# Performance work log

Hardware: AMD Instinct MI355X
Metric: run time of the kernel (lower is better)

The kernel has to match this reference:

```python
import jax, jax.numpy as jnp
import numpy as np
from math import factorial, sqrt

L_MAX = 3
MUL = 64
# e3nn FullyConnectedTensorProduct instruction order: lexicographic over (l1, l2, l3)
# keeping paths with triangle inequality and matching parity ((-1)^(l1+l2) == (-1)^l3).
PATHS = [(l1, l2, l3)
         for l1 in range(L_MAX + 1)
         for l2 in range(L_MAX + 1)
         for l3 in range(L_MAX + 1)
         if abs(l1 - l2) <= l3 <= l1 + l2 and (l1 + l2 + l3) % 2 == 0]
assert len(PATHS) == 23
N_TO = {l3: sum(1 for p in PATHS if p[2] == l3) for l3 in range(L_MAX + 1)}


def _su2_cg(j1, m1, j2, m2, j3, m3):
    # Complex-basis Clebsch-Gordan coefficient (Racah formula), as in e3nn.
    if m3 != m1 + m2:
        return 0.0
    f = factorial
    vmin = max(-j1 + j2 + m3, -j1 + m1, 0)
    vmax = min(j2 + j3 + m1, j3 - j1 + j2, j3 + m3)
    c = sqrt((2 * j3 + 1) * f(j3 + j1 - j2) * f(j3 - j1 + j2) * f(j1 + j2 - j3)
             * f(j3 + m3) * f(j3 - m3)
             / (f(j1 + j2 + j3 + 1) * f(j1 - m1) * f(j1 + m1) * f(j2 - m2) * f(j2 + m2)))
    s = 0.0
    for v in range(vmin, vmax + 1):
        s += (-1) ** (v + j2 + m2) / f(v) * f(j2 + j3 + m1 - v) * f(j1 - m1 + v) \
             / f(j3 - j1 + j2 - v) / f(j3 + m3 - v) / f(v + j1 - j2 - m3)
    return c * s


def _q(l):
    # Change of basis real -> complex spherical harmonics (e3nn convention).
    q = np.zeros((2 * l + 1, 2 * l + 1), dtype=np.complex128)
    for m in range(-l, 0):
        q[l + m, l + abs(m)] = 1.0 / np.sqrt(2.0)
        q[l + m, l - abs(m)] = -1j / np.sqrt(2.0)
    q[l, l] = 1.0
    for m in range(1, l + 1):
        q[l + m, l + abs(m)] = (-1) ** m / np.sqrt(2.0)
        q[l + m, l - abs(m)] = 1j * (-1) ** m / np.sqrt(2.0)
    return (-1j) ** l * q


def _w3j(l1, l2, l3):
    # Real-basis Wigner 3j tensor, unit Frobenius norm (e3nn's o3.wigner_3j).
    csu2 = np.zeros((2 * l1 + 1, 2 * l2 + 1, 2 * l3 + 1))
    for m1 in range(-l1, l1 + 1):
        for m2 in range(-l2, l2 + 1):
            m3 = m1 + m2
            if -l3 <= m3 <= l3:
                csu2[l1 + m1, l2 + m2, l3 + m3] = _su2_cg(l1, m1, l2, m2, l3, m3)
    q1, q2, q3 = _q(l1), _q(l2), _q(l3)
    c = np.einsum('ij,kl,mn,ikn->jlm', q1, q2, np.conj(q3.T), csu2.astype(np.complex128))
    c = np.real(c)
    return (c / np.linalg.norm(c)).astype(np.float32)


W3J = {p: jnp.asarray(_w3j(*p)) for p in PATHS}
# e3nn 'component' irrep_normalization + 'element' path_normalization:
# per-path coeff = sqrt(ir_out.dim / (n_paths_into_out * mul1 * mul2)).
COEFF = {p: float(np.sqrt((2 * p[2] + 1) / (N_TO[p[2]] * MUL * MUL))) for p in PATHS}


def setup_inputs():
    key = jax.random.key(0)
    kx, kw = jax.random.split(key)
    x = jax.random.normal(kx, (2, 1024, MUL * (L_MAX + 1) ** 2), dtype=jnp.float32)
    weights = jax.random.normal(kw, (len(PATHS), MUL, MUL, MUL), dtype=jnp.float32)
    return {"x": x, "weights": weights}


def reference(x, weights):
    B, N, D = x.shape
    Z = B * N
    xf = x.reshape(Z, D)
    # e3nn layout: blocks of (mul, 2l+1) concatenated over l; offset = MUL * l^2.
    xs = [xf[:, MUL * l * l: MUL * (l + 1) ** 2].reshape(Z, MUL, 2 * l + 1)
          for l in range(L_MAX + 1)]
    acc = [jnp.zeros((Z, MUL, 2 * l + 1), dtype=x.dtype) for l in range(L_MAX + 1)]
    for p, (l1, l2, l3) in enumerate(PATHS):
        c = W3J[(l1, l2, l3)]
        t1 = jnp.einsum('zui,ijk->zujk', xs[l1], c)            # [Z,u,2l2+1,2l3+1]
        t2 = jnp.einsum('zujk,zvj->zuvk', t1, xs[l2])          # [Z,u,v,2l3+1]
        seg = jnp.einsum('zuvk,uvw->zwk', t2, weights[p]) * COEFF[(l1, l2, l3)]
        acc[l3] = acc[l3] + seg
    out = jnp.concatenate([a.reshape(Z, -1) for a in acc], axis=-1)
    return out.reshape(B, N, -1)
```

## Files before the change

kernel.cpp:

```cpp
#include <hip/hip_runtime.h>

struct CD { double re, im; };
constexpr CD cmul(CD a, CD b){ return CD{a.re*b.re - a.im*b.im, a.re*b.im + a.im*b.re}; }
constexpr CD conj_(CD a){ return CD{a.re, -a.im}; }

constexpr double factd(int n){ double r = 1.0; for(int i = 2; i <= n; ++i) r *= (double)i; return r; }
constexpr double csqrt_(double x){
  if (x <= 0.0) return 0.0;
  double g = x > 1.0 ? x : 1.0;
  for (int i = 0; i < 100; ++i) g = 0.5*(g + x/g);
  return g;
}

constexpr double su2_cg(int j1,int m1,int j2,int m2,int j3,int m3){
  if (m3 != m1 + m2) return 0.0;
  int vmin = -j1 + j2 + m3;
  if (-j1 + m1 > vmin) vmin = -j1 + m1;
  if (0 > vmin) vmin = 0;
  int vmax = j2 + j3 + m1;
  if (j3 - j1 + j2 < vmax) vmax = j3 - j1 + j2;
  if (j3 + m3 < vmax) vmax = j3 + m3;
  double c = csqrt_((2.0*j3 + 1.0) * factd(j3 + j1 - j2) * factd(j3 - j1 + j2) * factd(j1 + j2 - j3)
                    * factd(j3 + m3) * factd(j3 - m3)
                    / (factd(j1 + j2 + j3 + 1) * factd(j1 - m1) * factd(j1 + m1)
                       * factd(j2 - m2) * factd(j2 + m2)));
  double s = 0.0;
  for (int v = vmin; v <= vmax; ++v){
    double t = (((v + j2 + m2) & 1) ? -1.0 : 1.0) / factd(v)
               * factd(j2 + j3 + m1 - v) * factd(j1 - m1 + v)
               / factd(j3 - j1 + j2 - v) / factd(j3 + m3 - v) / factd(v + j1 - j2 - m3);
    s += t;
  }
  return c * s;
}

struct QM { CD m[7][7]; };
constexpr QM qmat(int l){
  QM q{};
  double is2 = 1.0 / csqrt_(2.0);
  for (int mm = -l; mm < 0; ++mm){
    q.m[l+mm][l-mm] = CD{is2, 0.0};
    q.m[l+mm][l+mm] = CD{0.0, -is2};
  }
  q.m[l][l] = CD{1.0, 0.0};
  for (int mm = 1; mm <= l; ++mm){
    double sgn = (mm & 1) ? -1.0 : 1.0;
    q.m[l+mm][l+mm] = CD{sgn*is2, 0.0};
    q.m[l+mm][l-mm] = CD{0.0, sgn*is2};
  }
  CD ph = (l % 4 == 0) ? CD{1,0} : (l % 4 == 1) ? CD{0,-1} : (l % 4 == 2) ? CD{-1,0} : CD{0,1};
  for (int r = 0; r < 7; ++r)
    for (int c = 0; c < 7; ++c)
      q.m[r][c] = cmul(ph, q.m[r][c]);
  return q;
}

template<int L1,int L2,int L3> struct W3JT { float v[2*L1+1][2*L2+1][2*L3+1]; };

template<int L1,int L2,int L3>
constexpr W3JT<L1,L2,L3> make_w3j(){
  constexpr int D1 = 2*L1+1, D2 = 2*L2+1, D3 = 2*L3+1;
  QM q1 = qmat(L1), q2 = qmat(L2), q3 = qmat(L3);
  double cg[7][7] = {};
  for (int i = 0; i < D1; ++i)
    for (int k = 0; k < D2; ++k){
      int n = i + k - L1 - L2 + L3;
      if (n >= 0 && n < D3) cg[i][k] = su2_cg(L1, i-L1, L2, k-L2, L3, (i-L1)+(k-L2));
    }
  double c[D1][D2][D3] = {};
  double norm2 = 0.0;
  for (int j = 0; j < D1; ++j)
    for (int l = 0; l < D2; ++l)
      for (int m = 0; m < D3; ++m){
        CD s{0.0, 0.0};
        for (int i = 0; i < D1; ++i)
          for (int k = 0; k < D2; ++k){
            double g = cg[i][k];
            if (g == 0.0) continue;
            int n = i + k - L1 - L2 + L3;
            CD t = cmul(q1.m[i][j], q2.m[k][l]);
            t = cmul(t, conj_(q3.m[n][m]));
            s.re += t.re * g; s.im += t.im * g;
          }
        c[j][l][m] = s.re;
        norm2 += s.re * s.re;
      }
  double inv = 1.0 / csqrt_(norm2);
  W3JT<L1,L2,L3> w{};
  for (int j = 0; j < D1; ++j)
    for (int l = 0; l < D2; ++l)
      for (int m = 0; m < D3; ++m){
        double val = c[j][l][m] * inv;
        if (val < 1e-10 && val > -1e-10) val = 0.0;
        w.v[j][l][m] = (float)val;
      }
  return w;
}

__device__ __constant__ int L3P_[23]  = {0,1,2,3,1,0,2,1,3,2,2,1,3,0,2,1,3,3,2,1,3,0,2};
__device__ __constant__ int SWAPP_[23] = {0,1,1,1,0,0,0,1,1,1,0,0,0,0,0,1,1,0,0,0,0,0,0};
constexpr int K3CUM[24] = {0,1,4,9,16,19,20,25,28,35,40,45,48,55,56,61,64,71,78,83,86,93,94,99};
constexpr size_t ZW = 2048ull * 64ull;

typedef __bf16 bf16x8 __attribute__((ext_vector_type(8)));
typedef float  f32x4  __attribute__((ext_vector_type(4)));
typedef float  f32x2  __attribute__((ext_vector_type(2)));

__global__ void pack_w_kernel(const float* __restrict__ w, unsigned short* __restrict__ wp, int total){
  int idx = blockIdx.x * 256 + threadIdx.x;
  if (idx >= total) return;
  int e    = idx & 7;
  int lane = (idx >> 3) & 63;
  int nt   = (idx >> 9) & 3;
  int hf   = (idx >> 11) & 1;
  int s    = (idx >> 12) & 63;
  int p    = idx >> 18;
  int kv = hf*32 + (lane >> 4)*8 + e;
  int wc = nt*16 + (lane & 15);
  int l3 = L3P_[p];
  const float nto[4] = {4.f, 6.f, 7.f, 6.f};
  float coeff = sqrtf((2.f*l3 + 1.f) / (nto[l3] * 4096.f));
  int a = SWAPP_[p] ? kv : s;
  int b = SWAPP_[p] ? s : kv;
  float val = w[(((size_t)p*64 + a)*64 + b)*64 + wc] * coeff;
  unsigned bits = __builtin_bit_cast(unsigned, val);
  unsigned r = (bits + 0x7FFFu + ((bits >> 16) & 1u)) >> 16;
  wp[idx] = (unsigned short)r;
}

__global__ void transpose_x(const float* __restrict__ x, float* __restrict__ xT){
  __shared__ float t[32][33];
  int bx = blockIdx.x, by = blockIdx.y;
  int tx = threadIdx.x & 31, ty = threadIdx.x >> 5;
  #pragma unroll
  for (int r = 0; r < 4; ++r)
    t[ty + r*8][tx] = x[(size_t)(by*32 + ty + r*8)*1024 + bx*32 + tx];
  __syncthreads();
  #pragma unroll
  for (int r = 0; r < 4; ++r)
    xT[(size_t)(bx*32 + ty + r*8)*2048 + by*32 + tx] = t[tx][ty + r*8];
}

template<int P,int L1,int L2,int L3,bool SWAP,int G0,int G,bool PART>
__device__ __forceinline__ void run_slot(
    int tile, const float* __restrict__ xT,
    const unsigned short* __restrict__ wp,
    float* __restrict__ dst, float* red)
{
  constexpr int K3 = 2*L3+1;
  constexpr int LK = SWAP ? L1 : L2;
  constexpr int LS = SWAP ? L2 : L1;
  constexpr int DK = 2*LK+1, DS = 2*LS+1;
  constexpr auto C = make_w3j<L1,L2,L3>();

  const int lane = threadIdx.x & 63;
  const int wv   = threadIdx.x >> 6;
  const int zc   = tile*16 + (lane & 15);

  f32x2 xk2[4][DK];
  {
    const float* xkb = xT + (size_t)(64*LK*LK)*2048 + zc;
    const int t0 = wv*32 + (lane >> 4)*8;
    #pragma unroll
    for (int q = 0; q < 4; ++q)
      #pragma unroll
      for (int t = 0; t < DK; ++t){
        float lo = xkb[(size_t)((t0 + 2*q    )*DK + t)*2048];
        float hi = xkb[(size_t)((t0 + 2*q + 1)*DK + t)*2048];
        xk2[q][t] = f32x2{lo, hi};
      }
  }

  const float* xsb = xT + (size_t)(64*LS*LS)*2048 + zc;
  const unsigned short* wu = wp + (size_t)P*262144 + (size_t)wv*2048 + (size_t)lane*8;

  f32x4 acc[G][4];
  #pragma unroll
  for (int a = 0; a < G; ++a)
    #pragma unroll
    for (int b = 0; b < 4; ++b) acc[a][b] = f32x4{0.f,0.f,0.f,0.f};

  const float* xsp = xsb;
  float xs[DS];
  #pragma unroll
  for (int j = 0; j < DS; ++j) xs[j] = xsp[(size_t)j*2048];

  for (int s = 0; s < 64; ++s){
    bf16x8 bfrag[4];
    #pragma unroll
    for (int nt = 0; nt < 4; ++nt)
      bfrag[nt] = *reinterpret_cast<const bf16x8*>(wu + nt*512);

    const float* xnp = (s < 63) ? xsp + (size_t)DS*2048 : xsp;
    float xn[DS];
    #pragma unroll
    for (int j = 0; j < DS; ++j) xn[j] = xnp[(size_t)j*2048];

    #pragma unroll
    for (int kk = 0; kk < G; ++kk){
      float dk[DK];
      #pragma unroll
      for (int t = 0; t < DK; ++t) dk[t] = 0.f;
      #pragma unroll
      for (int t = 0; t < DK; ++t){
        #pragma unroll
        for (int j = 0; j < DS; ++j){
          const float cv = SWAP ? C.v[t][j][G0+kk] : C.v[j][t][G0+kk];
          if (cv != 0.0f) dk[t] = __builtin_fmaf(xs[j], cv, dk[t]);
        }
      }
      f32x2 af2[4];
      #pragma unroll
      for (int q = 0; q < 4; ++q) af2[q] = f32x2{0.f, 0.f};
      #pragma unroll
      for (int t = 0; t < DK; ++t){
        const f32x2 d2 = f32x2{dk[t], dk[t]};
        #pragma unroll
        for (int q = 0; q < 4; ++q)
          af2[q] += xk2[q][t] * d2;
      }
      bf16x8 af;
      #pragma unroll
      for (int q = 0; q < 4; ++q){
        af[2*q]   = (__bf16)af2[q].x;
        af[2*q+1] = (__bf16)af2[q].y;
      }
      __builtin_amdgcn_s_setprio(1);
      #pragma unroll
      for (int nt = 0; nt < 4; ++nt)
        acc[kk][nt] = __builtin_amdgcn_mfma_f32_16x16x32_bf16(af, bfrag[nt], acc[kk][nt], 0, 0, 0);
      __builtin_amdgcn_s_setprio(0);
    }
    #pragma unroll
    for (int j = 0; j < DS; ++j) xs[j] = xn[j];
    xsp += (size_t)DS*2048;
    wu  += 4096;
  }

  constexpr int Gh = (G + 1) / 2;
  static_assert(Gh <= 3, "red[] sized for Gh<=3");
  auto store_one = [&](int kk, int nt, const f32x4& o, const f32x4& a){
    #pragma unroll
    for (int r = 0; r < 4; ++r){
      int zl = ((lane >> 4) << 2) + r;
      int wc = nt*16 + (lane & 15);
      float val = a[r] + o[r];
      if constexpr (PART){
        dst[(size_t)K3CUM[P]*ZW + (size_t)(tile*16 + zl)*(64*K3) + wc*K3 + (G0+kk)] = val;
      } else {
        unsafeAtomicAdd(dst + (size_t)(tile*16 + zl)*1024 + 64*L3*L3 + wc*K3 + (G0+kk), val);
      }
    }
  };

  if (wv == 1){
    #pragma unroll
    for (int kk = 0; kk < Gh; ++kk)
      #pragma unroll
      for (int nt = 0; nt < 4; ++nt)
        *reinterpret_cast<f32x4*>(&red[((kk*4 + nt)*64 + lane)*4]) = acc[kk][nt];
  }
  __syncthreads();
  if (wv == 0){
    #pragma unroll
    for (int kk = 0; kk < Gh; ++kk)
      #pragma unroll
      for (int nt = 0; nt < 4; ++nt){
        f32x4 o = *reinterpret_cast<const f32x4*>(&red[((kk*4 + nt)*64 + lane)*4]);
        store_one(kk, nt, o, acc[kk][nt]);
      }
  }
  if constexpr (G > Gh){
    if (wv == 0){
      #pragma unroll
      for (int kk = Gh; kk < G; ++kk)
        #pragma unroll
        for (int nt = 0; nt < 4; ++nt)
          *reinterpret_cast<f32x4*>(&red[(((kk-Gh)*4 + nt)*64 + lane)*4]) = acc[kk][nt];
    }
    __syncthreads();
    if (wv == 1){
      #pragma unroll
      for (int kk = Gh; kk < G; ++kk)
        #pragma unroll
        for (int nt = 0; nt < 4; ++nt){
          f32x4 o = *reinterpret_cast<const f32x4*>(&red[(((kk-Gh)*4 + nt)*64 + lane)*4]);
          store_one(kk, nt, o, acc[kk][nt]);
        }
    }
  }
}

template<bool PART>
__global__ __launch_bounds__(128, 3) void tp_main(const float* __restrict__ xT,
    const unsigned short* __restrict__ wp, float* __restrict__ dst)
{
  __shared__ __align__(16) float red[3072];
  const int slot = blockIdx.x >> 7;
  const int tile = blockIdx.x & 127;
  switch (slot){
    case 0:  run_slot< 6,1,1,2,false,0,5,PART>(tile,xT,wp,dst,red); break;
    case 1:  run_slot<16,2,3,3,true ,0,3,PART>(tile,xT,wp,dst,red); break;
    case 2:  run_slot<20,3,2,3,false,0,3,PART>(tile,xT,wp,dst,red); break;
    case 3:  run_slot<14,2,2,2,false,0,3,PART>(tile,xT,wp,dst,red); break;
    case 4:  run_slot<15,2,3,1,true ,0,3,PART>(tile,xT,wp,dst,red); break;
    case 5:  run_slot<19,3,2,1,false,0,3,PART>(tile,xT,wp,dst,red); break;
    case 6:  run_slot< 8,1,2,3,true ,0,4,PART>(tile,xT,wp,dst,red); break;
    case 7:  run_slot<12,2,1,3,false,0,4,PART>(tile,xT,wp,dst,red); break;
    case 8:  run_slot<22,3,3,2,false,0,2,PART>(tile,xT,wp,dst,red); break;
    case 9:  run_slot<22,3,3,2,false,2,2,PART>(tile,xT,wp,dst,red); break;
    case 10: run_slot< 9,1,3,2,true ,0,3,PART>(tile,xT,wp,dst,red); break;
    case 11: run_slot<16,2,3,3,true ,3,2,PART>(tile,xT,wp,dst,red); break;
    case 12: run_slot<16,2,3,3,true ,5,2,PART>(tile,xT,wp,dst,red); break;
    case 13: run_slot<20,3,2,3,false,3,2,PART>(tile,xT,wp,dst,red); break;
    case 14: run_slot<20,3,2,3,false,5,2,PART>(tile,xT,wp,dst,red); break;
    case 15: run_slot< 2,0,2,2,true ,0,5,PART>(tile,xT,wp,dst,red); break;
    case 16: run_slot<10,2,0,2,false,0,5,PART>(tile,xT,wp,dst,red); break;
    case 17: run_slot<11,2,1,1,false,0,3,PART>(tile,xT,wp,dst,red); break;
    case 18: run_slot< 7,1,2,1,true ,0,3,PART>(tile,xT,wp,dst,red); break;
    case 19: run_slot<18,3,1,2,false,0,3,PART>(tile,xT,wp,dst,red); break;
    case 20: run_slot< 8,1,2,3,true ,4,3,PART>(tile,xT,wp,dst,red); break;
    case 21: run_slot<12,2,1,3,false,4,3,PART>(tile,xT,wp,dst,red); break;
    case 22: run_slot<14,2,2,2,false,3,2,PART>(tile,xT,wp,dst,red); break;
    case 23: run_slot< 9,1,3,2,true ,3,2,PART>(tile,xT,wp,dst,red); break;
    case 24: run_slot<18,3,1,2,false,3,2,PART>(tile,xT,wp,dst,red); break;
    case 25: run_slot<22,3,3,2,false,4,1,PART>(tile,xT,wp,dst,red); break;
    case 26: run_slot<21,3,3,0,false,0,1,PART>(tile,xT,wp,dst,red); break;
    case 27: run_slot< 3,0,3,3,true ,0,4,PART>(tile,xT,wp,dst,red); break;
    case 28: run_slot<17,3,0,3,false,0,4,PART>(tile,xT,wp,dst,red); break;
    case 29: run_slot< 3,0,3,3,true ,4,3,PART>(tile,xT,wp,dst,red); break;
    case 30: run_slot<17,3,0,3,false,4,3,PART>(tile,xT,wp,dst,red); break;
    case 31: run_slot< 1,0,1,1,true ,0,3,PART>(tile,xT,wp,dst,red); break;
    case 32: run_slot< 4,1,0,1,false,0,3,PART>(tile,xT,wp,dst,red); break;
    case 33: run_slot<13,2,2,0,false,0,1,PART>(tile,xT,wp,dst,red); break;
    case 34: run_slot< 5,1,1,0,false,0,1,PART>(tile,xT,wp,dst,red); break;
    case 35: run_slot< 0,0,0,0,false,0,1,PART>(tile,xT,wp,dst,red); break;
    default: break;
  }
}

__global__ void gather_out(const float* __restrict__ part, float* __restrict__ out){
  int gid = blockIdx.x * 256 + threadIdx.x;
  int z = gid >> 10, j = gid & 1023;
  float s;
  if (j < 64){
    size_t b = (size_t)z*64 + j;
    s = part[(size_t)K3CUM[0]*ZW + b] + part[(size_t)K3CUM[5]*ZW + b]
      + part[(size_t)K3CUM[13]*ZW + b] + part[(size_t)K3CUM[21]*ZW + b];
  } else if (j < 256){
    size_t b = (size_t)z*192 + (j - 64);
    s = part[(size_t)K3CUM[1]*ZW + b] + part[(size_t)K3CUM[4]*ZW + b]
      + part[(size_t)K3CUM[7]*ZW + b] + part[(size_t)K3CUM[11]*ZW + b]
      + part[(size_t)K3CUM[15]*ZW + b] + part[(size_t)K3CUM[19]*ZW + b];
  } else if (j < 576){
    size_t b = (size_t)z*320 + (j - 256);
    s = part[(size_t)K3CUM[2]*ZW + b] + part[(size_t)K3CUM[6]*ZW + b]
      + part[(size_t)K3CUM[9]*ZW + b] + part[(size_t)K3CUM[10]*ZW + b]
      + part[(size_t)K3CUM[14]*ZW + b] + part[(size_t)K3CUM[18]*ZW + b]
      + part[(size_t)K3CUM[22]*ZW + b];
  } else {
    size_t b = (size_t)z*448 + (j - 576);
    s = part[(size_t)K3CUM[3]*ZW + b] + part[(size_t)K3CUM[8]*ZW + b]
      + part[(size_t)K3CUM[12]*ZW + b] + part[(size_t)K3CUM[16]*ZW + b]
      + part[(size_t)K3CUM[17]*ZW + b] + part[(size_t)K3CUM[20]*ZW + b];
  }
  out[gid] = s;
}

extern "C" void kernel_launch(void* const* d_in, const int* in_sizes, int n_in,
                              void* d_out, int out_size, void* d_ws, size_t ws_size,
                              hipStream_t stream)
{
  const float* x = (const float*)d_in[0];
  const float* w = (const float*)d_in[1];
  float* out = (float*)d_out;

  const size_t packB = 23ull*64*2*4*64*8 * sizeof(unsigned short);
  const size_t xTB   = 1024ull*2048*sizeof(float);
  const size_t partB = 99ull*ZW*sizeof(float);
  const int totalW = 23*64*2*4*64*8;

  unsigned short* wp = (unsigned short*)d_ws;
  float* xT   = (float*)((char*)d_ws + packB);
  float* part = (float*)((char*)d_ws + packB + xTB);

  if (ws_size < packB + xTB) return;

  pack_w_kernel<<<(totalW + 255)/256, 256, 0, stream>>>(w, wp, totalW);
  dim3 tg(32, 64);
  transpose_x<<<tg, 256, 0, stream>>>(x, xT);

  if (ws_size >= packB + xTB + partB){
    tp_main<true><<<36*128, 128, 0, stream>>>(xT, wp, part);
    gather_out<<<(2048*1024)/256, 256, 0, stream>>>(part, out);
  } else {
    hipMemsetAsync(d_out, 0, (size_t)out_size * sizeof(float), stream);
    tp_main<false><<<36*128, 128, 0, stream>>>(xT, wp, out);
  }
}
```

Before: 203.5 us.

## Split main kernel into fat and lean launches with G<=2 slots

New measurement: 246.8 us. 1.21x slower.

```diff
diff --git a/kernel.cpp b/kernel.cpp
--- a/kernel.cpp
+++ b/kernel.cpp
@@ -152,6 +152,7 @@
   constexpr int LS = SWAP ? L2 : L1;
   constexpr int DK = 2*LK+1, DS = 2*LS+1;
   constexpr auto C = make_w3j<L1,L2,L3>();
+  static_assert(G <= 2, "acc/red sized for G<=2");
 
   const int lane = threadIdx.x & 63;
   const int wv   = threadIdx.x >> 6;
@@ -237,8 +238,6 @@
     wu  += 4096;
   }
 
-  constexpr int Gh = (G + 1) / 2;
-  static_assert(Gh <= 3, "red[] sized for Gh<=3");
   auto store_one = [&](int kk, int nt, const f32x4& o, const f32x4& a){
     #pragma unroll
     for (int r = 0; r < 4; ++r){
@@ -253,88 +252,107 @@
     }
   };
 
-  if (wv == 1){
-    #pragma unroll
-    for (int kk = 0; kk < Gh; ++kk)
+  #pragma unroll
+  for (int ph = 0; ph < G; ++ph){
+    const int writer = ph & 1;
+    if (wv == writer){
       #pragma unroll
       for (int nt = 0; nt < 4; ++nt)
-        *reinterpret_cast<f32x4*>(&red[((kk*4 + nt)*64 + lane)*4]) = acc[kk][nt];
-  }
-  __syncthreads();
-  if (wv == 0){
-    #pragma unroll
-    for (int kk = 0; kk < Gh; ++kk)
-      #pragma unroll
-      for (int nt = 0; nt < 4; ++nt){
-        f32x4 o = *reinterpret_cast<const f32x4*>(&red[((kk*4 + nt)*64 + lane)*4]);
-        store_one(kk, nt, o, acc[kk][nt]);
-      }
-  }
-  if constexpr (G > Gh){
-    if (wv == 0){
-      #pragma unroll
-      for (int kk = Gh; kk < G; ++kk)
-        #pragma unroll
-        for (int nt = 0; nt < 4; ++nt)
-          *reinterpret_cast<f32x4*>(&red[(((kk-Gh)*4 + nt)*64 + lane)*4]) = acc[kk][nt];
+        *reinterpret_cast<f32x4*>(&red[(nt*64 + lane)*4]) = acc[ph][nt];
     }
     __syncthreads();
-    if (wv == 1){
-      #pragma unroll
-      for (int kk = Gh; kk < G; ++kk)
-        #pragma unroll
-        for (int nt = 0; nt < 4; ++nt){
-          f32x4 o = *reinterpret_cast<const f32x4*>(&red[(((kk-Gh)*4 + nt)*64 + lane)*4]);
-          store_one(kk, nt, o, acc[kk][nt]);
-        }
+    if (wv != writer){
+      #pragma unroll
+      for (int nt = 0; nt < 4; ++nt){
+        f32x4 o = *reinterpret_cast<const f32x4*>(&red[(nt*64 + lane)*4]);
+        store_one(ph, nt, o, acc[ph][nt]);
+      }
     }
+    if (ph + 1 < G) __syncthreads();
   }
 }
 
 template<bool PART>
-__global__ __launch_bounds__(128, 3) void tp_main(const float* __restrict__ xT,
+__global__ __launch_bounds__(128, 3) void tp_fat(const float* __restrict__ xT,
     const unsigned short* __restrict__ wp, float* __restrict__ dst)
 {
-  __shared__ __align__(16) float red[3072];
+  __shared__ __align__(16) float red[1024];
   const int slot = blockIdx.x >> 7;
   const int tile = blockIdx.x & 127;
   switch (slot){
-    case 0:  run_slot< 6,1,1,2,false,0,5,PART>(tile,xT,wp,dst,red); break;
-    case 1:  run_slot<16,2,3,3,true ,0,3,PART>(tile,xT,wp,dst,red); break;
-    case 2:  run_slot<20,3,2,3,false,0,3,PART>(tile,xT,wp,dst,red); break;
-    case 3:  run_slot<14,2,2,2,false,0,3,PART>(tile,xT,wp,dst,red); break;
-    case 4:  run_slot<15,2,3,1,true ,0,3,PART>(tile,xT,wp,dst,red); break;
-    case 5:  run_slot<19,3,2,1,false,0,3,PART>(tile,xT,wp,dst,red); break;
-    case 6:  run_slot< 8,1,2,3,true ,0,4,PART>(tile,xT,wp,dst,red); break;
-    case 7:  run_slot<12,2,1,3,false,0,4,PART>(tile,xT,wp,dst,red); break;
-    case 8:  run_slot<22,3,3,2,false,0,2,PART>(tile,xT,wp,dst,red); break;
-    case 9:  run_slot<22,3,3,2,false,2,2,PART>(tile,xT,wp,dst,red); break;
-    case 10: run_slot< 9,1,3,2,true ,0,3,PART>(tile,xT,wp,dst,red); break;
-    case 11: run_slot<16,2,3,3,true ,3,2,PART>(tile,xT,wp,dst,red); break;
-    case 12: run_slot<16,2,3,3,true ,5,2,PART>(tile,xT,wp,dst,red); break;
-    case 13: run_slot<20,3,2,3,false,3,2,PART>(tile,xT,wp,dst,red); break;
-    case 14: run_slot<20,3,2,3,false,5,2,PART>(tile,xT,wp,dst,red); break;
-    case 15: run_slot< 2,0,2,2,true ,0,5,PART>(tile,xT,wp,dst,red); break;
-    case 16: run_slot<10,2,0,2,false,0,5,PART>(tile,xT,wp,dst,red); break;
-    case 17: run_slot<11,2,1,1,false,0,3,PART>(tile,xT,wp,dst,red); break;
-    case 18: run_slot< 7,1,2,1,true ,0,3,PART>(tile,xT,wp,dst,red); break;
-    case 19: run_slot<18,3,1,2,false,0,3,PART>(tile,xT,wp,dst,red); break;
-    case 20: run_slot< 8,1,2,3,true ,4,3,PART>(tile,xT,wp,dst,red); break;
-    case 21: run_slot<12,2,1,3,false,4,3,PART>(tile,xT,wp,dst,red); break;
-    case 22: run_slot<14,2,2,2,false,3,2,PART>(tile,xT,wp,dst,red); break;
-    case 23: run_slot< 9,1,3,2,true ,3,2,PART>(tile,xT,wp,dst,red); break;
-    case 24: run_slot<18,3,1,2,false,3,2,PART>(tile,xT,wp,dst,red); break;
-    case 25: run_slot<22,3,3,2,false,4,1,PART>(tile,xT,wp,dst,red); break;
-    case 26: run_slot<21,3,3,0,false,0,1,PART>(tile,xT,wp,dst,red); break;
-    case 27: run_slot< 3,0,3,3,true ,0,4,PART>(tile,xT,wp,dst,red); break;
-    case 28: run_slot<17,3,0,3,false,0,4,PART>(tile,xT,wp,dst,red); break;
-    case 29: run_slot< 3,0,3,3,true ,4,3,PART>(tile,xT,wp,dst,red); break;
-    case 30: run_slot<17,3,0,3,false,4,3,PART>(tile,xT,wp,dst,red); break;
-    case 31: run_slot< 1,0,1,1,true ,0,3,PART>(tile,xT,wp,dst,red); break;
-    case 32: run_slot< 4,1,0,1,false,0,3,PART>(tile,xT,wp,dst,red); break;
-    case 33: run_slot<13,2,2,0,false,0,1,PART>(tile,xT,wp,dst,red); break;
-    case 34: run_slot< 5,1,1,0,false,0,1,PART>(tile,xT,wp,dst,red); break;
-    case 35: run_slot< 0,0,0,0,false,0,1,PART>(tile,xT,wp,dst,red); break;
+    case 0:  run_slot<22,3,3,2,false,0,2,PART>(tile,xT,wp,dst,red); break;
+    case 1:  run_slot<22,3,3,2,false,2,2,PART>(tile,xT,wp,dst,red); break;
+    case 2:  run_slot<22,3,3,2,false,4,1,PART>(tile,xT,wp,dst,red); break;
+    case 3:  run_slot<16,2,3,3,true ,0,2,PART>(tile,xT,wp,dst,red); break;
+    case 4:  run_slot<16,2,3,3,true ,2,2,PART>(tile,xT,wp,dst,red); break;
+    case 5:  run_slot<16,2,3,3,true ,4,2,PART>(tile,xT,wp,dst,red); break;
+    case 6:  run_slot<16,2,3,3,true ,6,1,PART>(tile,xT,wp,dst,red); break;
+    case 7:  run_slot<20,3,2,3,false,0,2,PART>(tile,xT,wp,dst,red); break;
+    case 8:  run_slot<20,3,2,3,false,2,2,PART>(tile,xT,wp,dst,red); break;
+    case 9:  run_slot<20,3,2,3,false,4,2,PART>(tile,xT,wp,dst,red); break;
+    case 10: run_slot<20,3,2,3,false,6,1,PART>(tile,xT,wp,dst,red); break;
+    case 11: run_slot<15,2,3,1,true ,0,2,PART>(tile,xT,wp,dst,red); break;
+    case 12: run_slot<15,2,3,1,true ,2,1,PART>(tile,xT,wp,dst,red); break;
+    case 13: run_slot<19,3,2,1,false,0,2,PART>(tile,xT,wp,dst,red); break;
+    case 14: run_slot<19,3,2,1,false,2,1,PART>(tile,xT,wp,dst,red); break;
+    case 15: run_slot<14,2,2,2,false,0,2,PART>(tile,xT,wp,dst,red); break;
+    case 16: run_slot<14,2,2,2,false,2,2,PART>(tile,xT,wp,dst,red); break;
+    case 17: run_slot<14,2,2,2,false,4,1,PART>(tile,xT,wp,dst,red); break;
+    case 18: run_slot<21,3,3,0,false,0,1,PART>(tile,xT,wp,dst,red); break;
+    case 19: run_slot<13,2,2,0,false,0,1,PART>(tile,xT,wp,dst,red); break;
+    default: break;
+  }
+}
+
+template<bool PART>
+__global__ __launch_bounds__(128, 4) void tp_lean(const float* __restrict__ xT,
+    const unsigned short* __restrict__ wp, float* __restrict__ dst)
+{
+  __shared__ __align__(16) float red[1024];
+  const int slot = blockIdx.x >> 7;
+  const int tile = blockIdx.x & 127;
+  switch (slot){
+    case 0:  run_slot< 8,1,2,3,true ,0,2,PART>(tile,xT,wp,dst,red); break;
+    case 1:  run_slot< 8,1,2,3,true ,2,2,PART>(tile,xT,wp,dst,red); break;
+    case 2:  run_slot< 8,1,2,3,true ,4,2,PART>(tile,xT,wp,dst,red); break;
+    case 3:  run_slot< 8,1,2,3,true ,6,1,PART>(tile,xT,wp,dst,red); break;
+    case 4:  run_slot< 9,1,3,2,true ,0,2,PART>(tile,xT,wp,dst,red); break;
+    case 5:  run_slot< 9,1,3,2,true ,2,2,PART>(tile,xT,wp,dst,red); break;
+    case 6:  run_slot< 9,1,3,2,true ,4,1,PART>(tile,xT,wp,dst,red); break;
+    case 7:  run_slot<18,3,1,2,false,0,2,PART>(tile,xT,wp,dst,red); break;
+    case 8:  run_slot<18,3,1,2,false,2,2,PART>(tile,xT,wp,dst,red); break;
+    case 9:  run_slot<18,3,1,2,false,4,1,PART>(tile,xT,wp,dst,red); break;
+    case 10: run_slot< 3,0,3,3,true ,0,2,PART>(tile,xT,wp,dst,red); break;
+    case 11: run_slot< 3,0,3,3,true ,2,2,PART>(tile,xT,wp,dst,red); break;
+    case 12: run_slot< 3,0,3,3,true ,4,2,PART>(tile,xT,wp,dst,red); break;
+    case 13: run_slot< 3,0,3,3,true ,6,1,PART>(tile,xT,wp,dst,red); break;
+    case 14: run_slot<17,3,0,3,false,0,2,PART>(tile,xT,wp,dst,red); break;
+    case 15: run_slot<17,3,0,3,false,2,2,PART>(tile,xT,wp,dst,red); break;
+    case 16: run_slot<17,3,0,3,false,4,2,PART>(tile,xT,wp,dst,red); break;
+    case 17: run_slot<17,3,0,3,false,6,1,PART>(tile,xT,wp,dst,red); break;
+    case 18: run_slot<12,2,1,3,false,0,2,PART>(tile,xT,wp,dst,red); break;
+    case 19: run_slot<12,2,1,3,false,2,2,PART>(tile,xT,wp,dst,red); break;
+    case 20: run_slot<12,2,1,3,false,4,2,PART>(tile,xT,wp,dst,red); break;
+    case 21: run_slot<12,2,1,3,false,6,1,PART>(tile,xT,wp,dst,red); break;
+    case 22: run_slot< 7,1,2,1,true ,0,2,PART>(tile,xT,wp,dst,red); break;
+    case 23: run_slot< 7,1,2,1,true ,2,1,PART>(tile,xT,wp,dst,red); break;
+    case 24: run_slot<11,2,1,1,false,0,2,PART>(tile,xT,wp,dst,red); break;
+    case 25: run_slot<11,2,1,1,false,2,1,PART>(tile,xT,wp,dst,red); break;
+    case 26: run_slot< 2,0,2,2,true ,0,2,PART>(tile,xT,wp,dst,red); break;
+    case 27: run_slot< 2,0,2,2,true ,2,2,PART>(tile,xT,wp,dst,red); break;
+    case 28: run_slot< 2,0,2,2,true ,4,1,PART>(tile,xT,wp,dst,red); break;
+    case 29: run_slot<10,2,0,2,false,0,2,PART>(tile,xT,wp,dst,red); break;
+    case 30: run_slot<10,2,0,2,false,2,2,PART>(tile,xT,wp,dst,red); break;
+    case 31: run_slot<10,2,0,2,false,4,1,PART>(tile,xT,wp,dst,red); break;
+    case 32: run_slot< 6,1,1,2,false,0,2,PART>(tile,xT,wp,dst,red); break;
+    case 33: run_slot< 6,1,1,2,false,2,2,PART>(tile,xT,wp,dst,red); break;
+    case 34: run_slot< 6,1,1,2,false,4,1,PART>(tile,xT,wp,dst,red); break;
+    case 35: run_slot< 1,0,1,1,true ,0,2,PART>(tile,xT,wp,dst,red); break;
+    case 36: run_slot< 1,0,1,1,true ,2,1,PART>(tile,xT,wp,dst,red); break;
+    case 37: run_slot< 4,1,0,1,false,0,2,PART>(tile,xT,wp,dst,red); break;
+    case 38: run_slot< 4,1,0,1,false,2,1,PART>(tile,xT,wp,dst,red); break;
+    case 39: run_slot< 5,1,1,0,false,0,1,PART>(tile,xT,wp,dst,red); break;
+    case 40: run_slot< 0,0,0,0,false,0,1,PART>(tile,xT,wp,dst,red); break;
     default: break;
   }
 }
@@ -391,10 +409,12 @@
   transpose_x<<<tg, 256, 0, stream>>>(x, xT);
 
   if (ws_size >= packB + xTB + partB){
-    tp_main<true><<<36*128, 128, 0, stream>>>(xT, wp, part);
+    tp_fat <true><<<20*128, 128, 0, stream>>>(xT, wp, part);
+    tp_lean<true><<<41*128, 128, 0, stream>>>(xT, wp, part);
     gather_out<<<(2048*1024)/256, 256, 0, stream>>>(part, out);
   } else {
     hipMemsetAsync(d_out, 0, (size_t)out_size * sizeof(float), stream);
-    tp_main<false><<<36*128, 128, 0, stream>>>(xT, wp, out);
-  }
-}
+    tp_fat <false><<<20*128, 128, 0, stream>>>(xT, wp, out);
+    tp_lean<false><<<41*128, 128, 0, stream>>>(xT, wp, out);
+  }
+}
```
